# Kernel tuning notes

Measured on AMD Instinct MI355X. Metric: run time of the kernel, lower is better.

The kernel has to match this reference:

```python
import jax, jax.numpy as jnp
import numpy as np

WS = 8   # window size
NH = 8   # num heads


def layernorm(x, g, b, eps=1e-5):
    m = jnp.mean(x, axis=-1, keepdims=True)
    v = jnp.var(x, axis=-1, keepdims=True)
    return (x - m) * jax.lax.rsqrt(v + eps) * g + b


def setup_inputs() -> dict:
    key = jax.random.key(0)
    ks = jax.random.split(key, 8)
    B, C, H, W = 16, 256, 64, 64
    s = 0.02
    inp = {
        "x": jax.random.normal(ks[0], (B, C, H, W), jnp.float32),
        "norm1_g": jnp.ones((C,), jnp.float32),
        "norm1_b": jnp.zeros((C,), jnp.float32),
        "qkv_w": jax.random.normal(ks[1], (3 * C, C), jnp.float32) * s,
        "qkv_b": jnp.zeros((3 * C,), jnp.float32),
        "rel_bias_table": jax.random.normal(ks[2], ((2 * WS - 1) ** 2, NH), jnp.float32) * s,
        "proj_w": jax.random.normal(ks[3], (C, C), jnp.float32) * s,
        "proj_b": jnp.zeros((C,), jnp.float32),
        "norm2_g": jnp.ones((C,), jnp.float32),
        "norm2_b": jnp.zeros((C,), jnp.float32),
        "fc1_w": jax.random.normal(ks[4], (4 * C, C), jnp.float32) * s,
        "fc1_b": jnp.zeros((4 * C,), jnp.float32),
        "fc2_w": jax.random.normal(ks[5], (C, 4 * C), jnp.float32) * s,
        "fc2_b": jnp.zeros((C,), jnp.float32),
    }
    # relative position index (Swin standard), shape (WS*WS, WS*WS), int constant
    coords = np.stack(np.meshgrid(np.arange(WS), np.arange(WS), indexing="ij")).reshape(2, -1)
    rel = (coords[:, :, None] - coords[:, None, :]).transpose(1, 2, 0)
    rel[:, :, 0] += WS - 1
    rel[:, :, 1] += WS - 1
    rel[:, :, 0] *= 2 * WS - 1
    inp["rel_index"] = jnp.asarray(rel.sum(-1), jnp.int32)
    return inp


def reference(x, norm1_g, norm1_b, qkv_w, qkv_b, rel_bias_table, proj_w, proj_b,
              norm2_g, norm2_b, fc1_w, fc1_b, fc2_w, fc2_b, rel_index):
    B, C, H, W = x.shape
    N = WS * WS
    hd = C // NH
    scale = hd ** -0.5

    xs = jnp.transpose(x, (0, 2, 3, 1)).reshape(B, H * W, C)  # b (h w) c
    shortcut = xs

    y = layernorm(xs, norm1_g, norm1_b).reshape(B, H, W, C)
    # window partition -> (B*nW, N, C); shift_size = 0 (default), no cyclic shift / mask
    y = y.reshape(B, H // WS, WS, W // WS, WS, C).transpose(0, 1, 3, 2, 4, 5).reshape(-1, N, C)

    qkv = (y @ qkv_w.T + qkv_b).reshape(-1, N, 3, NH, hd).transpose(2, 0, 3, 1, 4)
    q, k, v = qkv[0], qkv[1], qkv[2]  # each (nW*B, NH, N, hd)

    attn = jnp.einsum("whnd,whmd->whnm", q * scale, k)
    bias = rel_bias_table[rel_index].transpose(2, 0, 1)  # (NH, N, N)
    attn = jax.nn.softmax(attn + bias[None], axis=-1)
    out = jnp.einsum("whnm,whmd->whnd", attn, v).transpose(0, 2, 1, 3).reshape(-1, N, C)
    out = out @ proj_w.T + proj_b

    # window reverse -> (B, H*W, C)
    out = out.reshape(B, H // WS, W // WS, WS, WS, C).transpose(0, 1, 3, 2, 4, 5).reshape(B, H * W, C)

    xs = shortcut + out
    h = layernorm(xs, norm2_g, norm2_b)
    h = jax.nn.gelu(h @ fc1_w.T + fc1_b, approximate=False) @ fc2_w.T + fc2_b
    xs = xs + h

    return jnp.transpose(xs.reshape(B, H, W, C), (0, 3, 1, 2))
```

## Files before the change

kernel.cpp:

```cpp
#include <hip/hip_runtime.h>

typedef unsigned short u16;
typedef __attribute__((ext_vector_type(8))) short short8;
typedef __attribute__((ext_vector_type(4))) float f32x4;

#define MFMA16(a, b, c) __builtin_amdgcn_mfma_f32_16x16x32_bf16((a), (b), (c), 0, 0, 0)
#define WAITV(N) asm volatile("s_waitcnt vmcnt(" #N ")" ::: "memory")
#define BARS() __builtin_amdgcn_s_barrier()
#define MFENCE() asm volatile("" ::: "memory")

__device__ __forceinline__ u16 f2b(float f) {
  unsigned b = __float_as_uint(f);
  b += 0x7FFFu + ((b >> 16) & 1u);
  return (u16)(b >> 16);
}
__device__ __forceinline__ float b2f(u16 u) { return __uint_as_float(((unsigned)u) << 16); }

__device__ __forceinline__ void gload_lds16(const void* g, void* l) {
  __builtin_amdgcn_global_load_lds((const __attribute__((address_space(1))) void*)g,
                                   (__attribute__((address_space(3))) void*)l, 16, 0, 0);
}

__device__ __forceinline__ float fast_gelu(float x) {
  const float u = x * 0.70710678118654752f;
  const float au = fabsf(u);
  float d = 1.f + 0.3275911f * au;
  float tt;
  asm("v_rcp_f32 %0, %1" : "=v"(tt) : "v"(d));
  float p = 1.061405429f * tt - 1.453152027f;
  p = p * tt + 1.421413741f;
  p = p * tt - 0.284496736f;
  p = p * tt + 0.254829592f;
  p = p * tt;
  const float e = __expf(-u * u);
  const float erf_au = 1.f - p * e;
  return 0.5f * x * (1.f + copysignf(erf_au, x));
}

__global__ __launch_bounds__(256) void prep_kernel(
    const float* __restrict__ qkv_w, const float* __restrict__ proj_w,
    const float* __restrict__ fc1_w, const float* __restrict__ fc2_w,
    const float* __restrict__ tbl, const int* __restrict__ ridx,
    u16* __restrict__ wqkv, u16* __restrict__ wproj, u16* __restrict__ wfc1,
    u16* __restrict__ wfc2, float* __restrict__ bfull) {
  int i = blockIdx.x * 256 + threadIdx.x;
  if (i < 196608) {
    wqkv[i] = f2b(qkv_w[i]);
  } else if (i < 262144) {
    wproj[i - 196608] = f2b(proj_w[i - 196608]);
  } else if (i < 524288) {
    wfc1[i - 262144] = f2b(fc1_w[i - 262144]);
  } else if (i < 786432) {
    wfc2[i - 524288] = f2b(fc2_w[i - 524288]);
  } else {
    int j = i - 786432;
    int hm = j >> 12, nm = j & 4095;
    bfull[j] = tbl[ridx[nm] * 8 + hm];
  }
}

__global__ __launch_bounds__(256) void ln1_win_kernel(const float* __restrict__ x,
                                                      const float* __restrict__ g,
                                                      const float* __restrict__ b,
                                                      u16* __restrict__ y,
                                                      u16* __restrict__ xsb) {
  __shared__ float red[2][4][64];
  const int bh = blockIdx.x;
  const int bb = bh >> 6, h = bh & 63;
  const int w = threadIdx.x & 63, cg = threadIdx.x >> 6;
  const float* xp = x + (size_t)bb * 1048576 + (size_t)h * 64 + w;
  float vals[64];
  float s = 0.f, ss = 0.f;
#pragma unroll
  for (int j = 0; j < 64; ++j) {
    float v = xp[(size_t)(cg * 64 + j) * 4096];
    vals[j] = v;
    s += v;
    ss += v * v;
  }
  red[0][cg][w] = s;
  red[1][cg][w] = ss;
  __syncthreads();
  const float S = red[0][0][w] + red[0][1][w] + red[0][2][w] + red[0][3][w];
  const float Q = red[1][0][w] + red[1][1][w] + red[1][2][w] + red[1][3][w];
  const float m = S * (1.f / 256.f);
  const float rstd = rsqrtf(Q * (1.f / 256.f) - m * m + 1e-5f);
  const int win = bb * 64 + ((h >> 3) << 3) + (w >> 3);
  const int tok = ((h & 7) << 3) + (w & 7);
  const size_t base = (size_t)win * 16384 + tok * 256 + cg * 64;
#pragma unroll
  for (int jj = 0; jj < 8; ++jj) {
    short8 o, raw;
#pragma unroll
    for (int q = 0; q < 8; ++q) {
      const int c64 = jj * 8 + q;
      const int c = cg * 64 + c64;
      raw[q] = (short)f2b(vals[c64]);
      o[q] = (short)f2b((vals[c64] - m) * rstd * g[c] + b[c]);
    }
    *(short8*)&y[base + jj * 8] = o;
    *(short8*)&xsb[base + jj * 8] = raw;
  }
}

template <int EPI, int KT, int NNT>
__global__ __launch_bounds__(256, 3) void gemm_bt(const u16* __restrict__ A,
                                                  const u16* __restrict__ W,
                                                  const float* __restrict__ bias,
                                                  u16* __restrict__ outh,
                                                  float* __restrict__ outf,
                                                  const u16* __restrict__ aux) {
  constexpr int NTK = KT >> 5;
  constexpr int NC = NNT * 128;
  __shared__ __align__(16) u16 As[3][4096];
  __shared__ __align__(16) u16 Bs[3][4096];
  const int xcd = blockIdx.x & 7, ii = blockIdx.x >> 3;
  const int mt = xcd * 64 + ii / NNT;
  const int nt = ii % NNT;
  const int tid = threadIdx.x;
  const int wv = tid >> 6, lane = tid & 63;
  const int wr = (wv >> 1) << 6;
  const int wc = (wv & 1) << 6;
  const int lrow4 = lane >> 2;
  const int srcslot = (((lane & 3) ^ ((lane >> 3) & 3)) << 3);
  const int lr = lane & 15, lg = lane >> 4;
  const int kq = ((lg ^ ((lr >> 1) & 3)) << 3);
  f32x4 acc[4][4];
#pragma unroll
  for (int mi = 0; mi < 4; ++mi)
#pragma unroll
    for (int ni = 0; ni < 4; ++ni) acc[mi][ni] = (f32x4){0.f, 0.f, 0.f, 0.f};
  const u16* Ab = A + (size_t)mt * 128 * KT;
  const u16* Wb = W + (size_t)nt * 128 * KT;

#define STG(BF, T)                                                                      \
  {                                                                                     \
    const int kt_ = (T) << 5;                                                           \
    _Pragma("unroll") for (int i_ = 0; i_ < 2; ++i_) {                                  \
      const int row_ = i_ * 64 + wv * 16 + lrow4;                                       \
      const int lo_ = i_ * 2048 + wv * 512;                                             \
      gload_lds16(Ab + (size_t)row_ * KT + kt_ + srcslot, &As[BF][lo_]);                \
      gload_lds16(Wb + (size_t)row_ * KT + kt_ + srcslot, &Bs[BF][lo_]);                \
    }                                                                                   \
  }
#define CMPT(BF)                                                                        \
  {                                                                                     \
    short8 a_[4], b_[4];                                                                \
    _Pragma("unroll") for (int mi = 0; mi < 4; ++mi)                                    \
        a_[mi] = *(const short8*)&As[BF][(wr + mi * 16 + lr) * 32 + kq];                \
    _Pragma("unroll") for (int ni = 0; ni < 4; ++ni)                                    \
        b_[ni] = *(const short8*)&Bs[BF][(wc + ni * 16 + lr) * 32 + kq];                \
    __builtin_amdgcn_s_setprio(1);                                                      \
    _Pragma("unroll") for (int mi = 0; mi < 4; ++mi)                                    \
        _Pragma("unroll") for (int ni = 0; ni < 4; ++ni)                                \
            acc[mi][ni] = MFMA16(a_[mi], b_[ni], acc[mi][ni]);                          \
    __builtin_amdgcn_s_setprio(0);                                                      \
  }

  STG(0, 0);
  STG(1, 1);
  STG(2, 2);
  int rr = 0;
  for (int t = 0; t < NTK; ++t) {
    if (t + 2 < NTK) {
      WAITV(8);
    } else if (t + 1 < NTK) {
      WAITV(4);
    } else {
      WAITV(0);
    }
    BARS();
    MFENCE();
    CMPT(rr);
    MFENCE();
    BARS();
    if (t + 3 < NTK) STG(rr, t + 3);
    rr = (rr == 2) ? 0 : rr + 1;
  }
#undef STG
#undef CMPT

  const int row0 = mt * 128 + wr + lg * 4;
  const int col0 = nt * 128 + wc + lr;

  if constexpr (EPI == 0) {
#pragma unroll
    for (int mi = 0; mi < 4; ++mi)
#pragma unroll
      for (int ni = 0; ni < 4; ++ni) {
        const int col = col0 + ni * 16;
        const int which = col >> 8, cc = col & 255;
        u16* dst = outh + (size_t)which * 16777216ull;
        const float scl = (which == 0) ? 0.17677669529663689f : 1.0f;
        const float bv = bias[col];
#pragma unroll
        for (int r = 0; r < 4; ++r) {
          const int row = row0 + mi * 16 + r;
          dst[(size_t)row * 256 + cc] = f2b((acc[mi][ni][r] + bv) * scl);
        }
      }
  } else if constexpr (EPI == 2) {
#pragma unroll
    for (int mi = 0; mi < 4; ++mi)
#pragma unroll
      for (int ni = 0; ni < 4; ++ni) {
        const int col = col0 + ni * 16;
        const float bv = bias[col];
#pragma unroll
        for (int r = 0; r < 4; ++r) {
          const int row = row0 + mi * 16 + r;
          outh[(size_t)row * NC + col] = f2b(fast_gelu(acc[mi][ni][r] + bv));
        }
      }
  } else {
#pragma unroll
    for (int mi = 0; mi < 4; ++mi)
#pragma unroll
      for (int ni = 0; ni < 4; ++ni) {
        const int col = col0 + ni * 16;
        const float bv = bias[col];
        const int row = row0 + mi * 16;
        const int win = row >> 6, tk = row & 63;
        const int bb = win >> 6;
        const int h = (((win >> 3) & 7) << 3) + (tk >> 3);
        const int w = ((win & 7) << 3) + (tk & 7);
        f32x4 v;
#pragma unroll
        for (int r = 0; r < 4; ++r)
          v[r] = acc[mi][ni][r] + bv + b2f(aux[(size_t)(row + r) * 256 + col]);
        *(f32x4*)&outf[(((size_t)bb * 256 + col) * 64 + h) * 64 + w] = v;
      }
  }
}

__global__ __launch_bounds__(512, 4) void proj_ln2(const u16* __restrict__ A,
                                                   const u16* __restrict__ W,
                                                   const float* __restrict__ bias,
                                                   const u16* __restrict__ xsb,
                                                   const float* __restrict__ g2,
                                                   const float* __restrict__ b2,
                                                   u16* __restrict__ xs2b,
                                                   u16* __restrict__ h2) {
  __shared__ __align__(16) u16 As[3][4096];
  __shared__ __align__(16) u16 Bs[3][8192];
  __shared__ float redS[4][128], redQ[4][128];
  const int mt = blockIdx.x;
  const int tid = threadIdx.x;
  const int wv = tid >> 6, lane = tid & 63;
  const int wm = wv >> 2, wn = wv & 3;
  const int rowa = tid >> 2;
  const int esl = (((tid & 3) ^ ((tid >> 3) & 3)) << 3);
  const int lr = lane & 15, lg = lane >> 4;
  const int kq = ((lg ^ ((lr >> 1) & 3)) << 3);
  f32x4 acc[4][4];
#pragma unroll
  for (int mi = 0; mi < 4; ++mi)
#pragma unroll
    for (int ni = 0; ni < 4; ++ni) acc[mi][ni] = (f32x4){0.f, 0.f, 0.f, 0.f};
  const u16* Ab = A + (size_t)mt * 128 * 256;

#define STG(BF, T)                                                                      \
  {                                                                                     \
    const int kt_ = (T) << 5;                                                           \
    gload_lds16(Ab + (size_t)rowa * 256 + kt_ + esl, &As[BF][tid * 8]);                 \
    gload_lds16(W + (size_t)rowa * 256 + kt_ + esl, &Bs[BF][tid * 8]);                  \
    gload_lds16(W + (size_t)(rowa + 128) * 256 + kt_ + esl, &Bs[BF][tid * 8 + 4096]);   \
  }
#define CMPT(BF)                                                                        \
  {                                                                                     \
    short8 a_[4], b_[4];                                                                \
    _Pragma("unroll") for (int mi = 0; mi < 4; ++mi)                                    \
        a_[mi] = *(const short8*)&As[BF][(wm * 64 + mi * 16 + lr) * 32 + kq];           \
    _Pragma("unroll") for (int ni = 0; ni < 4; ++ni)                                    \
        b_[ni] = *(const short8*)&Bs[BF][(wn * 64 + ni * 16 + lr) * 32 + kq];           \
    __builtin_amdgcn_s_setprio(1);                                                      \
    _Pragma("unroll") for (int mi = 0; mi < 4; ++mi)                                    \
        _Pragma("unroll") for (int ni = 0; ni < 4; ++ni)                                \
            acc[mi][ni] = MFMA16(a_[mi], b_[ni], acc[mi][ni]);                          \
    __builtin_amdgcn_s_setprio(0);                                                      \
  }

  STG(0, 0);
  STG(1, 1);
  STG(2, 2);
  int rr = 0;
  for (int t = 0; t < 8; ++t) {
    if (t + 2 < 8) {
      WAITV(6);
    } else if (t + 1 < 8) {
      WAITV(3);
    } else {
      WAITV(0);
    }
    BARS();
    MFENCE();
    CMPT(rr);
    MFENCE();
    BARS();
    if (t + 3 < 8) STG(rr, t + 3);
    rr = (rr == 2) ? 0 : rr + 1;
  }
#undef STG
#undef CMPT

  const int row0 = mt * 128 + wm * 64 + lg * 4;
  const int col0 = wn * 64 + lr;

#pragma unroll
  for (int mi = 0; mi < 4; ++mi)
#pragma unroll
    for (int ni = 0; ni < 4; ++ni) {
      const int col = col0 + ni * 16;
      const float bv = bias[col];
#pragma unroll
      for (int r = 0; r < 4; ++r)
        acc[mi][ni][r] += bv + b2f(xsb[(size_t)(row0 + mi * 16 + r) * 256 + col]);
    }
#pragma unroll
  for (int mi = 0; mi < 4; ++mi)
#pragma unroll
    for (int r = 0; r < 4; ++r) {
      float s = acc[mi][0][r] + acc[mi][1][r] + acc[mi][2][r] + acc[mi][3][r];
      float q = acc[mi][0][r] * acc[mi][0][r] + acc[mi][1][r] * acc[mi][1][r] +
                acc[mi][2][r] * acc[mi][2][r] + acc[mi][3][r] * acc[mi][3][r];
      s += __shfl_xor(s, 1); q += __shfl_xor(q, 1);
      s += __shfl_xor(s, 2); q += __shfl_xor(q, 2);
      s += __shfl_xor(s, 4); q += __shfl_xor(q, 4);
      s += __shfl_xor(s, 8); q += __shfl_xor(q, 8);
      if (lr == 0) {
        const int rl = wm * 64 + mi * 16 + lg * 4 + r;
        redS[wn][rl] = s;
        redQ[wn][rl] = q;
      }
    }
  __syncthreads();
#pragma unroll
  for (int mi = 0; mi < 4; ++mi)
#pragma unroll
    for (int r = 0; r < 4; ++r) {
      const int rl = wm * 64 + mi * 16 + lg * 4 + r;
      const float S = redS[0][rl] + redS[1][rl] + redS[2][rl] + redS[3][rl];
      const float Q = redQ[0][rl] + redQ[1][rl] + redQ[2][rl] + redQ[3][rl];
      const float m = S * (1.f / 256.f);
      const float rstd = rsqrtf(Q * (1.f / 256.f) - m * m + 1e-5f);
      const size_t row = row0 + mi * 16 + r;
#pragma unroll
      for (int ni = 0; ni < 4; ++ni) {
        const int col = col0 + ni * 16;
        const float v = acc[mi][ni][r];
        xs2b[row * 256 + col] = f2b(v);
        h2[row * 256 + col] = f2b((v - m) * rstd * g2[col] + b2[col]);
      }
    }
}

__global__ __launch_bounds__(64) void attn_kernel(const u16* __restrict__ qkv,
                                                  const float* __restrict__ biasf,
                                                  u16* __restrict__ aout) {
  __shared__ __align__(16) u16 sqk[5120];
  __shared__ __align__(16) u16 vt[2304];
  u16* qs = sqk;
  u16* ks = sqk + 2560;
  u16* pp = sqk;
  const int wh = blockIdx.x;
  const int head = wh & 7;
  const int win = wh >> 3;
  const int lane = threadIdx.x;
  const int lr = lane & 15, lg = lane >> 4;
  const size_t rbase = (size_t)win * 16384 + head * 32;
  const u16* qg = qkv + rbase;
  const u16* kg = qkv + 16777216ull + rbase;
  const u16* vg = qkv + 33554432ull + rbase;
#pragma unroll
  for (int i = 0; i < 4; ++i) {
    int ch = i * 64 + lane;
    int r = ch >> 2, qo = (ch & 3) * 8;
    *(short8*)&qs[r * 40 + qo] = *(const short8*)&qg[(size_t)r * 256 + qo];
    *(short8*)&ks[r * 40 + qo] = *(const short8*)&kg[(size_t)r * 256 + qo];
  }
  {
    short8 v0 = *(const short8*)&vg[(size_t)lane * 256];
    short8 v1 = *(const short8*)&vg[(size_t)lane * 256 + 8];
    short8 v2 = *(const short8*)&vg[(size_t)lane * 256 + 16];
    short8 v3 = *(const short8*)&vg[(size_t)lane * 256 + 24];
#pragma unroll
    for (int j = 0; j < 8; ++j) {
      vt[j * 72 + lane] = (u16)v0[j];
      vt[(8 + j) * 72 + lane] = (u16)v1[j];
      vt[(16 + j) * 72 + lane] = (u16)v2[j];
      vt[(24 + j) * 72 + lane] = (u16)v3[j];
    }
  }
  __syncthreads();
  f32x4 sf[4][4];
#pragma unroll
  for (int mi = 0; mi < 4; ++mi)
#pragma unroll
    for (int ni = 0; ni < 4; ++ni) sf[mi][ni] = (f32x4){0.f, 0.f, 0.f, 0.f};
  {
    short8 a[4], bq[4];
#pragma unroll
    for (int mi = 0; mi < 4; ++mi) a[mi] = *(const short8*)&qs[(mi * 16 + lr) * 40 + lg * 8];
#pragma unroll
    for (int ni = 0; ni < 4; ++ni) bq[ni] = *(const short8*)&ks[(ni * 16 + lr) * 40 + lg * 8];
#pragma unroll
    for (int mi = 0; mi < 4; ++mi)
#pragma unroll
      for (int ni = 0; ni < 4; ++ni) sf[mi][ni] = MFMA16(a[mi], bq[ni], sf[mi][ni]);
  }
  __syncthreads();
  const float* bh = biasf + (size_t)head * 4096;
#pragma unroll
  for (int mi = 0; mi < 4; ++mi) {
#pragma unroll
    for (int r = 0; r < 4; ++r) {
      const int n = mi * 16 + lg * 4 + r;
      float v0 = sf[mi][0][r] + bh[n * 64 + lr];
      float v1 = sf[mi][1][r] + bh[n * 64 + 16 + lr];
      float v2 = sf[mi][2][r] + bh[n * 64 + 32 + lr];
      float v3 = sf[mi][3][r] + bh[n * 64 + 48 + lr];
      float mx = fmaxf(fmaxf(v0, v1), fmaxf(v2, v3));
      mx = fmaxf(mx, __shfl_xor(mx, 1));
      mx = fmaxf(mx, __shfl_xor(mx, 2));
      mx = fmaxf(mx, __shfl_xor(mx, 4));
      mx = fmaxf(mx, __shfl_xor(mx, 8));
      float e0 = __expf(v0 - mx), e1 = __expf(v1 - mx);
      float e2 = __expf(v2 - mx), e3 = __expf(v3 - mx);
      float sm = e0 + e1 + e2 + e3;
      sm += __shfl_xor(sm, 1);
      sm += __shfl_xor(sm, 2);
      sm += __shfl_xor(sm, 4);
      sm += __shfl_xor(sm, 8);
      const float inv = 1.f / sm;
      pp[n * 72 + lr] = f2b(e0 * inv);
      pp[n * 72 + 16 + lr] = f2b(e1 * inv);
      pp[n * 72 + 32 + lr] = f2b(e2 * inv);
      pp[n * 72 + 48 + lr] = f2b(e3 * inv);
    }
  }
  __syncthreads();
  f32x4 o[4][2];
#pragma unroll
  for (int mi = 0; mi < 4; ++mi)
#pragma unroll
    for (int ni = 0; ni < 2; ++ni) o[mi][ni] = (f32x4){0.f, 0.f, 0.f, 0.f};
#pragma unroll
  for (int kk = 0; kk < 2; ++kk) {
    short8 pa[4], vb[2];
#pragma unroll
    for (int mi = 0; mi < 4; ++mi)
      pa[mi] = *(const short8*)&pp[(mi * 16 + lr) * 72 + kk * 32 + lg * 8];
#pragma unroll
    for (int ni = 0; ni < 2; ++ni)
      vb[ni] = *(const short8*)&vt[(ni * 16 + lr) * 72 + kk * 32 + lg * 8];
#pragma unroll
    for (int mi = 0; mi < 4; ++mi)
#pragma unroll
      for (int ni = 0; ni < 2; ++ni) o[mi][ni] = MFMA16(pa[mi], vb[ni], o[mi][ni]);
  }
  u16* op = aout + (size_t)win * 16384 + head * 32;
#pragma unroll
  for (int mi = 0; mi < 4; ++mi)
#pragma unroll
    for (int ni = 0; ni < 2; ++ni)
#pragma unroll
      for (int r = 0; r < 4; ++r) {
        const int n = mi * 16 + lg * 4 + r;
        op[(size_t)n * 256 + ni * 16 + lr] = f2b(o[mi][ni][r]);
      }
}

extern "C" void kernel_launch(void* const* d_in, const int* in_sizes, int n_in,
                              void* d_out, int out_size, void* d_ws, size_t ws_size,
                              hipStream_t stream) {
  const float* x = (const float*)d_in[0];
  const float* n1g = (const float*)d_in[1];
  const float* n1b = (const float*)d_in[2];
  const float* qkv_w = (const float*)d_in[3];
  const float* qkv_b = (const float*)d_in[4];
  const float* tbl = (const float*)d_in[5];
  const float* proj_w = (const float*)d_in[6];
  const float* proj_b = (const float*)d_in[7];
  const float* n2g = (const float*)d_in[8];
  const float* n2b = (const float*)d_in[9];
  const float* fc1_w = (const float*)d_in[10];
  const float* fc1_b = (const float*)d_in[11];
  const float* fc2_w = (const float*)d_in[12];
  const float* fc2_b = (const float*)d_in[13];
  const int* relidx = (const int*)d_in[14];
  float* outp = (float*)d_out;

  char* w = (char*)d_ws;
  const size_t Mi = 1ull << 20;
  if (ws_size < 237 * Mi) return;
  u16* Y = (u16*)(w + 0);
  u16* qb = (u16*)(w + 32 * Mi);
  u16* aout = (u16*)(w + 0);
  u16* xs2b = (u16*)(w + 0);
  u16* h2 = (u16*)(w + 32 * Mi);
  u16* xsb = (u16*)(w + 128 * Mi);
  u16* h1 = (u16*)(w + 64 * Mi);
  u16* wqkv = (u16*)(w + 192 * Mi);
  u16* wproj = wqkv + 196608;
  u16* wfc1 = wproj + 65536;
  u16* wfc2 = wfc1 + 262144;
  float* bfull = (float*)(w + 192 * Mi + 1572864);

  prep_kernel<<<3200, 256, 0, stream>>>(qkv_w, proj_w, fc1_w, fc2_w, tbl, relidx, wqkv,
                                        wproj, wfc1, wfc2, bfull);
  ln1_win_kernel<<<1024, 256, 0, stream>>>(x, n1g, n1b, Y, xsb);
  gemm_bt<0, 256, 6><<<3072, 256, 0, stream>>>(Y, wqkv, qkv_b, qb, nullptr, nullptr);
  attn_kernel<<<8192, 64, 0, stream>>>(qb, bfull, aout);
  proj_ln2<<<512, 512, 0, stream>>>(aout, wproj, proj_b, xsb, n2g, n2b, xs2b, h2);
  gemm_bt<2, 256, 8><<<4096, 256, 0, stream>>>(h2, wfc1, fc1_b, h1, nullptr, nullptr);
  gemm_bt<3, 1024, 2><<<1024, 256, 0, stream>>>(h1, wfc2, fc2_b, nullptr, outp, xs2b);
}
```

Measured before the change: 338.7 us.

## Switch GEMM to 32x32x16 MFMA, tanh-style GELU, packed bf16 converts

New measurement: 326.6 us. -3.6%, faster.

```diff
diff --git a/kernel.cpp b/kernel.cpp
--- a/kernel.cpp
+++ b/kernel.cpp
@@ -3,7 +3,9 @@
 typedef unsigned short u16;
 typedef __attribute__((ext_vector_type(8))) short short8;
 typedef __attribute__((ext_vector_type(4))) float f32x4;
-
+typedef __attribute__((ext_vector_type(16))) float f32x16;
+
+#define MFMA32(a, b, c) __builtin_amdgcn_mfma_f32_32x32x16_bf16((a), (b), (c), 0, 0, 0)
 #define MFMA16(a, b, c) __builtin_amdgcn_mfma_f32_16x16x32_bf16((a), (b), (c), 0, 0, 0)
 #define WAITV(N) asm volatile("s_waitcnt vmcnt(" #N ")" ::: "memory")
 #define BARS() __builtin_amdgcn_s_barrier()
@@ -16,25 +18,24 @@
 }
 __device__ __forceinline__ float b2f(u16 u) { return __uint_as_float(((unsigned)u) << 16); }
 
+__device__ __forceinline__ unsigned cvt2(float lo, float hi) {
+  unsigned r;
+  asm("v_cvt_pk_bf16_f32 %0, %1, %2" : "=v"(r) : "v"(lo), "v"(hi));
+  return r;
+}
+
 __device__ __forceinline__ void gload_lds16(const void* g, void* l) {
   __builtin_amdgcn_global_load_lds((const __attribute__((address_space(1))) void*)g,
                                    (__attribute__((address_space(3))) void*)l, 16, 0, 0);
 }
 
 __device__ __forceinline__ float fast_gelu(float x) {
-  const float u = x * 0.70710678118654752f;
-  const float au = fabsf(u);
-  float d = 1.f + 0.3275911f * au;
-  float tt;
-  asm("v_rcp_f32 %0, %1" : "=v"(tt) : "v"(d));
-  float p = 1.061405429f * tt - 1.453152027f;
-  p = p * tt + 1.421413741f;
-  p = p * tt - 0.284496736f;
-  p = p * tt + 0.254829592f;
-  p = p * tt;
-  const float e = __expf(-u * u);
-  const float erf_au = 1.f - p * e;
-  return 0.5f * x * (1.f + copysignf(erf_au, x));
+  const float x2 = x * x;
+  const float z = x * (1.5957691216f + 0.0713548162f * x2);
+  const float e = __expf(-z);
+  float r;
+  asm("v_rcp_f32 %0, %1" : "=v"(r) : "v"(1.f + e));
+  return x * r;
 }
 
 __global__ __launch_bounds__(256) void prep_kernel(
@@ -121,40 +122,43 @@
   const int wv = tid >> 6, lane = tid & 63;
   const int wr = (wv >> 1) << 6;
   const int wc = (wv & 1) << 6;
-  const int lrow4 = lane >> 2;
-  const int srcslot = (((lane & 3) ^ ((lane >> 3) & 3)) << 3);
-  const int lr = lane & 15, lg = lane >> 4;
-  const int kq = ((lg ^ ((lr >> 1) & 3)) << 3);
-  f32x4 acc[4][4];
-#pragma unroll
-  for (int mi = 0; mi < 4; ++mi)
-#pragma unroll
-    for (int ni = 0; ni < 4; ++ni) acc[mi][ni] = (f32x4){0.f, 0.f, 0.f, 0.f};
+  const int srow = tid >> 2;
+  const int sslot = (((tid & 3) ^ ((tid >> 5) & 3)) << 3);
+  const int l31 = lane & 31, lh = lane >> 5;
+  const int xk = (l31 >> 3) & 3;
+  f32x16 acc[2][2];
+#pragma unroll
+  for (int ti = 0; ti < 2; ++ti)
+#pragma unroll
+    for (int tj = 0; tj < 2; ++tj)
+#pragma unroll
+      for (int e = 0; e < 16; ++e) acc[ti][tj][e] = 0.f;
   const u16* Ab = A + (size_t)mt * 128 * KT;
   const u16* Wb = W + (size_t)nt * 128 * KT;
 
 #define STG(BF, T)                                                                      \
   {                                                                                     \
     const int kt_ = (T) << 5;                                                           \
-    _Pragma("unroll") for (int i_ = 0; i_ < 2; ++i_) {                                  \
-      const int row_ = i_ * 64 + wv * 16 + lrow4;                                       \
-      const int lo_ = i_ * 2048 + wv * 512;                                             \
-      gload_lds16(Ab + (size_t)row_ * KT + kt_ + srcslot, &As[BF][lo_]);                \
-      gload_lds16(Wb + (size_t)row_ * KT + kt_ + srcslot, &Bs[BF][lo_]);                \
-    }                                                                                   \
+    gload_lds16(Ab + (size_t)srow * KT + kt_ + sslot, &As[BF][tid * 8]);                \
+    gload_lds16(Ab + (size_t)(srow + 64) * KT + kt_ + sslot, &As[BF][2048 + tid * 8]);  \
+    gload_lds16(Wb + (size_t)srow * KT + kt_ + sslot, &Bs[BF][tid * 8]);                \
+    gload_lds16(Wb + (size_t)(srow + 64) * KT + kt_ + sslot, &Bs[BF][2048 + tid * 8]);  \
   }
 #define CMPT(BF)                                                                        \
   {                                                                                     \
-    short8 a_[4], b_[4];                                                                \
-    _Pragma("unroll") for (int mi = 0; mi < 4; ++mi)                                    \
-        a_[mi] = *(const short8*)&As[BF][(wr + mi * 16 + lr) * 32 + kq];                \
-    _Pragma("unroll") for (int ni = 0; ni < 4; ++ni)                                    \
-        b_[ni] = *(const short8*)&Bs[BF][(wc + ni * 16 + lr) * 32 + kq];                \
-    __builtin_amdgcn_s_setprio(1);                                                      \
-    _Pragma("unroll") for (int mi = 0; mi < 4; ++mi)                                    \
-        _Pragma("unroll") for (int ni = 0; ni < 4; ++ni)                                \
-            acc[mi][ni] = MFMA16(a_[mi], b_[ni], acc[mi][ni]);                          \
-    __builtin_amdgcn_s_setprio(0);                                                      \
+    short8 a_[2][2], b_[2][2];                                                          \
+    _Pragma("unroll") for (int ti = 0; ti < 2; ++ti)                                    \
+        _Pragma("unroll") for (int kk = 0; kk < 2; ++kk)                                \
+            a_[ti][kk] = *(const short8*)&As[BF][(wr + ti * 32 + l31) * 32 +            \
+                                                (((kk * 2 + lh) ^ xk) << 3)];           \
+    _Pragma("unroll") for (int tj = 0; tj < 2; ++tj)                                    \
+        _Pragma("unroll") for (int kk = 0; kk < 2; ++kk)                                \
+            b_[tj][kk] = *(const short8*)&Bs[BF][(wc + tj * 32 + l31) * 32 +            \
+                                                (((kk * 2 + lh) ^ xk) << 3)];           \
+    _Pragma("unroll") for (int kk = 0; kk < 2; ++kk)                                    \
+        _Pragma("unroll") for (int ti = 0; ti < 2; ++ti)                                \
+            _Pragma("unroll") for (int tj = 0; tj < 2; ++tj)                            \
+                acc[ti][tj] = MFMA32(a_[ti][kk], b_[tj][kk], acc[ti][tj]);              \
   }
 
   STG(0, 0);
@@ -180,55 +184,72 @@
 #undef STG
 #undef CMPT
 
-  const int row0 = mt * 128 + wr + lg * 4;
-  const int col0 = nt * 128 + wc + lr;
+  const int row0 = mt * 128 + wr + lh * 4;
+  const int colL = nt * 128 + wc + l31;
 
   if constexpr (EPI == 0) {
 #pragma unroll
-    for (int mi = 0; mi < 4; ++mi)
-#pragma unroll
-      for (int ni = 0; ni < 4; ++ni) {
-        const int col = col0 + ni * 16;
+    for (int ti = 0; ti < 2; ++ti)
+#pragma unroll
+      for (int tj = 0; tj < 2; ++tj) {
+        const int col = colL + tj * 32;
         const int which = col >> 8, cc = col & 255;
         u16* dst = outh + (size_t)which * 16777216ull;
         const float scl = (which == 0) ? 0.17677669529663689f : 1.0f;
         const float bv = bias[col];
 #pragma unroll
-        for (int r = 0; r < 4; ++r) {
-          const int row = row0 + mi * 16 + r;
-          dst[(size_t)row * 256 + cc] = f2b((acc[mi][ni][r] + bv) * scl);
+        for (int rg = 0; rg < 4; ++rg) {
+          const int rowb = row0 + ti * 32 + rg * 8;
+          const unsigned p01 = cvt2((acc[ti][tj][rg * 4 + 0] + bv) * scl,
+                                    (acc[ti][tj][rg * 4 + 1] + bv) * scl);
+          const unsigned p23 = cvt2((acc[ti][tj][rg * 4 + 2] + bv) * scl,
+                                    (acc[ti][tj][rg * 4 + 3] + bv) * scl);
+          dst[(size_t)(rowb + 0) * 256 + cc] = (u16)p01;
+          dst[(size_t)(rowb + 1) * 256 + cc] = (u16)(p01 >> 16);
+          dst[(size_t)(rowb + 2) * 256 + cc] = (u16)p23;
+          dst[(size_t)(rowb + 3) * 256 + cc] = (u16)(p23 >> 16);
         }
       }
   } else if constexpr (EPI == 2) {
 #pragma unroll
-    for (int mi = 0; mi < 4; ++mi)
-#pragma unroll
-      for (int ni = 0; ni < 4; ++ni) {
-        const int col = col0 + ni * 16;
+    for (int ti = 0; ti < 2; ++ti)
+#pragma unroll
+      for (int tj = 0; tj < 2; ++tj) {
+        const int col = colL + tj * 32;
         const float bv = bias[col];
 #pragma unroll
-        for (int r = 0; r < 4; ++r) {
-          const int row = row0 + mi * 16 + r;
-          outh[(size_t)row * NC + col] = f2b(fast_gelu(acc[mi][ni][r] + bv));
+        for (int rg = 0; rg < 4; ++rg) {
+          const int rowb = row0 + ti * 32 + rg * 8;
+          const unsigned p01 = cvt2(fast_gelu(acc[ti][tj][rg * 4 + 0] + bv),
+                                    fast_gelu(acc[ti][tj][rg * 4 + 1] + bv));
+          const unsigned p23 = cvt2(fast_gelu(acc[ti][tj][rg * 4 + 2] + bv),
+                                    fast_gelu(acc[ti][tj][rg * 4 + 3] + bv));
+          outh[(size_t)(rowb + 0) * NC + col] = (u16)p01;
+          outh[(size_t)(rowb + 1) * NC + col] = (u16)(p01 >> 16);
+          outh[(size_t)(rowb + 2) * NC + col] = (u16)p23;
+          outh[(size_t)(rowb + 3) * NC + col] = (u16)(p23 >> 16);
         }
       }
   } else {
 #pragma unroll
-    for (int mi = 0; mi < 4; ++mi)
-#pragma unroll
-      for (int ni = 0; ni < 4; ++ni) {
-        const int col = col0 + ni * 16;
+    for (int ti = 0; ti < 2; ++ti)
+#pragma unroll
+      for (int tj = 0; tj < 2; ++tj) {
+        const int col = colL + tj * 32;
         const float bv = bias[col];
-        const int row = row0 + mi * 16;
-        const int win = row >> 6, tk = row & 63;
-        const int bb = win >> 6;
-        const int h = (((win >> 3) & 7) << 3) + (tk >> 3);
-        const int w = ((win & 7) << 3) + (tk & 7);
-        f32x4 v;
-#pragma unroll
-        for (int r = 0; r < 4; ++r)
-          v[r] = acc[mi][ni][r] + bv + b2f(aux[(size_t)(row + r) * 256 + col]);
-        *(f32x4*)&outf[(((size_t)bb * 256 + col) * 64 + h) * 64 + w] = v;
+#pragma unroll
+        for (int rg = 0; rg < 4; ++rg) {
+          const int rowb = row0 + ti * 32 + rg * 8;
+          const int win = rowb >> 6, tk = rowb & 63;
+          const int bb = win >> 6;
+          const int h = (((win >> 3) & 7) << 3) + (tk >> 3);
+          const int w = ((win & 7) << 3) + (tk & 7);
+          f32x4 v;
+#pragma unroll
+          for (int rq = 0; rq < 4; ++rq)
+            v[rq] = acc[ti][tj][rg * 4 + rq] + bv + b2f(aux[(size_t)(rowb + rq) * 256 + col]);
+          *(f32x4*)&outf[(((size_t)bb * 256 + col) * 64 + h) * 64 + w] = v;
+        }
       }
   }
 }
@@ -273,11 +294,9 @@
         a_[mi] = *(const short8*)&As[BF][(wm * 64 + mi * 16 + lr) * 32 + kq];           \
     _Pragma("unroll") for (int ni = 0; ni < 4; ++ni)                                    \
         b_[ni] = *(const short8*)&Bs[BF][(wn * 64 + ni * 16 + lr) * 32 + kq];           \
-    __builtin_amdgcn_s_setprio(1);                                                      \
     _Pragma("unroll") for (int mi = 0; mi < 4; ++mi)                                    \
         _Pragma("unroll") for (int ni = 0; ni < 4; ++ni)                                \
             acc[mi][ni] = MFMA16(a_[mi], b_[ni], acc[mi][ni]);                          \
-    __builtin_amdgcn_s_setprio(0);                                                      \
   }
 
   STG(0, 0);
```
